# Kernel tuning notes

Measured on AMD Instinct MI355X. Metric: run time of the kernel, lower is better.

Reference implementation:

```python
import jax, jax.numpy as jnp
import numpy as np

WINDOWS = ((0, 8), (4, 12), (8, 16))  # DARM.SEG_WINDOWS
TOPK = 2                               # DARM.TOPK_SEG_PAIRS


def _l2norm(x, axis=-1, eps=1e-12):
    # torch F.normalize: x / max(||x||, eps)
    n = jnp.linalg.norm(x, axis=axis, keepdims=True)
    return x / jnp.maximum(n, eps)


def _segments(x):
    # x: [B, T, D] -> [B, W, L, D]
    return jnp.stack([x[:, s:e, :] for s, e in WINDOWS], axis=1)


def setup_inputs() -> dict:
    key = jax.random.key(0)
    k1, k2 = jax.random.split(key)
    n_way, n_shot, n_query, T, D = 10, 5, 400, 16, 1024
    support_features = jax.random.normal(k1, (n_way * n_shot, T, D), dtype=jnp.float32)
    query_features = jax.random.normal(k2, (n_query, T, D), dtype=jnp.float32)
    # init weights [0.5, 0.5] -> log -> softmax == softmax(zeros)
    fusion_logits = jnp.zeros((2,), dtype=jnp.float32)
    return {
        "support_features": support_features,
        "query_features": query_features,
        "fusion_logits": fusion_logits,
        "n_way": n_way,
        "n_shot": n_shot,
    }


def reference(support_features, query_features, fusion_logits, n_way, n_shot):
    # support_features: [C*K, T, D] with labels repeat(arange(C), K) (sorted, balanced)
    C, K = n_way, n_shot
    Q, T, D = query_features.shape
    inv_sqrt_d = 1.0 / np.sqrt(D).astype(np.float32)

    # ---- global branch: bi-MHM over class prototypes ----
    proto = support_features.reshape(C, K, T, D).mean(axis=1)          # [C, T, D]
    qn = _l2norm(query_features)                                       # [Q, T, D]
    pn = _l2norm(proto)                                                # [C, T, D]
    sim = jnp.einsum("qtd,csd->qcts", qn, pn)                          # [Q, C, T, T]
    dist = 1.0 - sim
    global_dist = dist.min(axis=3).sum(axis=2) + dist.min(axis=2).sum(axis=2)  # [Q, C]
    global_score = -global_dist

    # ---- segment branch ----
    sup_seg = _segments(support_features)                              # [C*K, W, L, D]
    q_seg = _segments(query_features)                                  # [Q, W, L, D]
    W, L = q_seg.shape[1], q_seg.shape[2]
    # group support by class: [C, W, K*L, D]
    cls_sup = sup_seg.reshape(C, K, W, L, D).transpose(0, 2, 1, 3, 4).reshape(C, W, K * L, D)

    sup_cond = _l2norm(cls_sup.mean(axis=2))                           # [C, W, D]
    q_cond = _l2norm(q_seg.mean(axis=2))                               # [Q, W, D]

    # attention-pool support tokens conditioned on each query segment mean
    s_scores = jnp.einsum("cwnd,qvd->qcvwn", cls_sup, q_cond) * inv_sqrt_d
    s_attn = jax.nn.softmax(s_scores, axis=-1)
    pooled_sup = jnp.einsum("qcvwn,cwnd->qcvwd", s_attn, cls_sup)      # [Q, C, W, W, D]
    # cosine(query_cond, pooled_sup); query_cond already unit norm
    score_s2q = jnp.einsum("qvd,qcvwd->qcvw", q_cond, _l2norm(pooled_sup))

    # attention-pool query tokens conditioned on each support segment mean
    q_scores = jnp.einsum("qvnd,cwd->qcvwn", q_seg, sup_cond) * inv_sqrt_d
    q_attn = jax.nn.softmax(q_scores, axis=-1)
    pooled_q = jnp.einsum("qcvwn,qvnd->qcvwd", q_attn, q_seg)          # [Q, C, W, W, D]
    score_q2s = jnp.einsum("qcvwd,cwd->qcvw", _l2norm(pooled_q), sup_cond)

    k = min(TOPK, W * W)
    top_s2q = jax.lax.top_k(score_s2q.reshape(Q, C, W * W), k)[0].mean(axis=-1)
    top_q2s = jax.lax.top_k(score_q2s.reshape(Q, C, W * W), k)[0].mean(axis=-1)
    segment_score = 0.5 * (top_s2q + top_q2s)                          # [Q, C]

    fusion = jax.nn.softmax(fusion_logits)
    final_logits = fusion[0] * global_score + fusion[1] * segment_score
    return final_logits
```

## Files before the change

### kernel.cpp

```cpp
#include <hip/hip_runtime.h>
#include <math.h>

#define C_WAY 10
#define K_SHOT 5
#define T_LEN 16
#define D_DIM 1024
#define NW 3
#define SEG_L 8

typedef __attribute__((ext_vector_type(8))) __bf16 bf16x8;
typedef __attribute__((ext_vector_type(4))) float f32x4;

static inline int cdiv(int a, int b) { return (a + b - 1) / b; }

__device__ __forceinline__ unsigned short f2bf(float f) {
    unsigned int u = __float_as_uint(f);
    u += 0x7fffu + ((u >> 16) & 1u);
    return (unsigned short)(u >> 16);
}
__device__ __forceinline__ float bf2f(unsigned short b) {
    return __uint_as_float(((unsigned int)b) << 16);
}
__device__ __forceinline__ ushort4 f2bf4(float4 v) {
    ushort4 b = {f2bf(v.x), f2bf(v.y), f2bf(v.z), f2bf(v.w)};
    return b;
}

__device__ __forceinline__ float wsum(float v) {
#pragma unroll
    for (int o = 32; o; o >>= 1) v += __shfl_xor(v, o);
    return v;
}
__device__ __forceinline__ float wmax(float v) {
#pragma unroll
    for (int o = 32; o; o >>= 1) v = fmaxf(v, __shfl_xor(v, o));
    return v;
}
__device__ __forceinline__ float wsum8(float v) {
#pragma unroll
    for (int o = 4; o; o >>= 1) v += __shfl_xor(v, o);
    return v;
}
__device__ __forceinline__ float wmax8(float v) {
#pragma unroll
    for (int o = 4; o; o >>= 1) v = fmaxf(v, __shfl_xor(v, o));
    return v;
}

__device__ __forceinline__ int cls_row(int i) {
    int c = i / 120, rem = i - c * 120;
    int w = rem / 40, tok = rem - w * 40;
    return c * 80 + (tok >> 3) * 16 + w * 4 + (tok & 7);
}
__device__ __forceinline__ int qseg_row(int m) {
    int q = m / 24, rem = m - q * 24;
    return q * 16 + (rem >> 3) * 4 + (rem & 7);
}

__global__ __launch_bounds__(256) void k_prep(const float* __restrict__ sup,
                                              const float* __restrict__ query,
                                              unsigned short* __restrict__ qbf,
                                              float* __restrict__ qrow_inv,
                                              unsigned short* __restrict__ qcondbf,
                                              unsigned short* __restrict__ supbf,
                                              unsigned short* __restrict__ protobf,
                                              float* __restrict__ pn_inv,
                                              unsigned short* __restrict__ scondbf,
                                              int Q) {
    __shared__ float red[NW][4];
    int b = blockIdx.x;
    int t = threadIdx.x, wv = t >> 6, lane = t & 63;
    if (b < Q) {
        int qq = b;
#pragma unroll
        for (int r0 = 0; r0 < 4; ++r0) {
            int row = qq * T_LEN + wv * 4 + r0;
            float sq = 0.f;
#pragma unroll
            for (int i = 0; i < 4; ++i) {
                float4 v = *(const float4*)&query[(size_t)row * D_DIM + (i * 64 + lane) * 4];
                *(ushort4*)&qbf[(size_t)row * D_DIM + (i * 64 + lane) * 4] = f2bf4(v);
                sq += v.x * v.x + v.y * v.y + v.z * v.z + v.w * v.w;
            }
            sq = wsum(sq);
            if (lane == 0) qrow_inv[row] = 1.0f / fmaxf(sqrtf(sq), 1e-12f);
        }
        __syncthreads();
        for (int v = 0; v < NW; ++v) {
            float4 acc = {0.f, 0.f, 0.f, 0.f};
#pragma unroll
            for (int l = 0; l < SEG_L; ++l) {
                ushort4 bb = *(const ushort4*)&qbf[((size_t)(qq * T_LEN + v * 4 + l)) * D_DIM + t * 4];
                acc.x += bf2f(bb.x); acc.y += bf2f(bb.y); acc.z += bf2f(bb.z); acc.w += bf2f(bb.w);
            }
            acc.x *= 0.125f; acc.y *= 0.125f; acc.z *= 0.125f; acc.w *= 0.125f;
            float sq = acc.x * acc.x + acc.y * acc.y + acc.z * acc.z + acc.w * acc.w;
            sq = wsum(sq);
            if (lane == 0) red[v][wv] = sq;
            __syncthreads();
            float tot = red[v][0] + red[v][1] + red[v][2] + red[v][3];
            float scl = 1.0f / fmaxf(sqrtf(tot), 1e-12f);
            float4 o = {acc.x * scl, acc.y * scl, acc.z * scl, acc.w * scl};
            *(ushort4*)&qcondbf[((size_t)(qq * NW + v)) * D_DIM + t * 4] = f2bf4(o);
            __syncthreads();
        }
    } else if (b < Q + C_WAY * K_SHOT) {
        int s = b - Q;
#pragma unroll
        for (int i = 0; i < 16; ++i) {
            int qd = i * 256 + t;
            float4 v = *(const float4*)&sup[(size_t)s * 16384 + qd * 4];
            *(ushort4*)&supbf[(size_t)s * 16384 + qd * 4] = f2bf4(v);
        }
    } else {
        int c = b - Q - C_WAY * K_SHOT;
#pragma unroll
        for (int r0 = 0; r0 < 4; ++r0) {
            int tt = wv * 4 + r0;
            float4 a[4] = {};
            for (int k = 0; k < K_SHOT; ++k)
#pragma unroll
                for (int i = 0; i < 4; ++i) {
                    float4 v = *(const float4*)&sup[((size_t)(c * 80 + k * 16 + tt)) * D_DIM + (i * 64 + lane) * 4];
                    a[i].x += v.x; a[i].y += v.y; a[i].z += v.z; a[i].w += v.w;
                }
            float sq = 0.f;
#pragma unroll
            for (int i = 0; i < 4; ++i) {
                a[i].x *= 0.2f; a[i].y *= 0.2f; a[i].z *= 0.2f; a[i].w *= 0.2f;
                sq += a[i].x * a[i].x + a[i].y * a[i].y + a[i].z * a[i].z + a[i].w * a[i].w;
            }
            sq = wsum(sq);
            if (lane == 0) pn_inv[c * T_LEN + tt] = 1.0f / fmaxf(sqrtf(sq), 1e-12f);
#pragma unroll
            for (int i = 0; i < 4; ++i)
                *(ushort4*)&protobf[((size_t)(c * T_LEN + tt)) * D_DIM + (i * 64 + lane) * 4] = f2bf4(a[i]);
        }
        if (wv < NW) {
            float4 a[4] = {};
            for (int k = 0; k < K_SHOT; ++k)
#pragma unroll
                for (int l = 0; l < SEG_L; ++l)
#pragma unroll
                    for (int i = 0; i < 4; ++i) {
                        float4 v = *(const float4*)&sup[((size_t)(c * 80 + k * 16 + wv * 4 + l)) * D_DIM + (i * 64 + lane) * 4];
                        a[i].x += v.x; a[i].y += v.y; a[i].z += v.z; a[i].w += v.w;
                    }
            float sq = 0.f;
            const float s = 1.0f / 40.0f;
#pragma unroll
            for (int i = 0; i < 4; ++i) {
                a[i].x *= s; a[i].y *= s; a[i].z *= s; a[i].w *= s;
                sq += a[i].x * a[i].x + a[i].y * a[i].y + a[i].z * a[i].z + a[i].w * a[i].w;
            }
            sq = wsum(sq);
            float scl = 1.0f / fmaxf(sqrtf(sq), 1e-12f);
#pragma unroll
            for (int i = 0; i < 4; ++i) {
                float4 o = {a[i].x * scl, a[i].y * scl, a[i].z * scl, a[i].w * scl};
                *(ushort4*)&scondbf[((size_t)(c * NW + wv)) * D_DIM + (i * 64 + lane) * 4] = f2bf4(o);
            }
        }
    }
}

template <int AM, int BM>
__device__ __forceinline__ void gemm_tile(const unsigned short* __restrict__ A,
                                          const unsigned short* __restrict__ B,
                                          float* __restrict__ Cb,
                                          int M, int N, int m0, int n0, int batch,
                                          unsigned short (&As)[64][72],
                                          unsigned short (&Bs)[64][72]) {
    int t = threadIdx.x;
    int srow = t >> 2, sk = (t & 3) * 8;
    long ga = -1, gb = -1;
    int am = m0 + srow;
    if (am < M) ga = (AM == 0) ? am : (AM == 1 ? qseg_row(am) : cls_row(batch * 40 + am));
    int bn = n0 + srow;
    if (bn < N) gb = (BM == 0) ? bn : (BM == 1 ? cls_row(bn) : cls_row(batch * 40 + bn));

    int w = t >> 6, l = t & 63;
    int rowbase = (w >> 1) * 32, colbase = (w & 1) * 32;
    int fr = l & 15, fc = l >> 4;

    f32x4 acc[2][2] = {};
    uint4 ra0 = {0, 0, 0, 0}, ra1 = {0, 0, 0, 0}, rb0 = {0, 0, 0, 0}, rb1 = {0, 0, 0, 0};
    if (ga >= 0) {
        ra0 = *(const uint4*)&A[(size_t)ga * D_DIM + sk];
        ra1 = *(const uint4*)&A[(size_t)ga * D_DIM + sk + 32];
    }
    if (gb >= 0) {
        rb0 = *(const uint4*)&B[(size_t)gb * D_DIM + sk];
        rb1 = *(const uint4*)&B[(size_t)gb * D_DIM + sk + 32];
    }
    for (int k0 = 0; k0 < D_DIM; k0 += 64) {
        __syncthreads();
        *(uint4*)&As[srow][sk] = ra0;
        *(uint4*)&As[srow][sk + 32] = ra1;
        *(uint4*)&Bs[srow][sk] = rb0;
        *(uint4*)&Bs[srow][sk + 32] = rb1;
        __syncthreads();
        int kn = k0 + 64;
        if (kn < D_DIM) {
            if (ga >= 0) {
                ra0 = *(const uint4*)&A[(size_t)ga * D_DIM + kn + sk];
                ra1 = *(const uint4*)&A[(size_t)ga * D_DIM + kn + sk + 32];
            }
            if (gb >= 0) {
                rb0 = *(const uint4*)&B[(size_t)gb * D_DIM + kn + sk];
                rb1 = *(const uint4*)&B[(size_t)gb * D_DIM + kn + sk + 32];
            }
        }
#pragma unroll
        for (int kk = 0; kk < 2; ++kk) {
            bf16x8 a0 = *(const bf16x8*)&As[rowbase + fr][kk * 32 + fc * 8];
            bf16x8 a1 = *(const bf16x8*)&As[rowbase + 16 + fr][kk * 32 + fc * 8];
            bf16x8 b0 = *(const bf16x8*)&Bs[colbase + fr][kk * 32 + fc * 8];
            bf16x8 b1 = *(const bf16x8*)&Bs[colbase + 16 + fr][kk * 32 + fc * 8];
            acc[0][0] = __builtin_amdgcn_mfma_f32_16x16x32_bf16(a0, b0, acc[0][0], 0, 0, 0);
            acc[0][1] = __builtin_amdgcn_mfma_f32_16x16x32_bf16(a0, b1, acc[0][1], 0, 0, 0);
            acc[1][0] = __builtin_amdgcn_mfma_f32_16x16x32_bf16(a1, b0, acc[1][0], 0, 0, 0);
            acc[1][1] = __builtin_amdgcn_mfma_f32_16x16x32_bf16(a1, b1, acc[1][1], 0, 0, 0);
        }
    }
    int crow = fc * 4, ccol = fr;
#pragma unroll
    for (int fi = 0; fi < 2; ++fi)
#pragma unroll
        for (int fj = 0; fj < 2; ++fj)
#pragma unroll
            for (int j = 0; j < 4; ++j) {
                int m = m0 + rowbase + fi * 16 + crow + j;
                int n = n0 + colbase + fj * 16 + ccol;
                if (m < M && n < N) Cb[(size_t)m * N + n] = acc[fi][fj][j];
            }
}

__global__ __launch_bounds__(256) void k_mega(const unsigned short* __restrict__ qbf,
                                              const unsigned short* __restrict__ protobf,
                                              const unsigned short* __restrict__ qcondbf,
                                              const unsigned short* __restrict__ supbf,
                                              const unsigned short* __restrict__ scondbf,
                                              float* __restrict__ SIM,
                                              float* __restrict__ Sraw,
                                              float* __restrict__ Qraw,
                                              float* __restrict__ Gsup,
                                              float* __restrict__ Gq,
                                              int Q, int mt0, int nb0, int mt1, int nb1,
                                              int nb2, int nb3) {
    __shared__ __align__(16) unsigned short As[64][72];
    __shared__ __align__(16) unsigned short Bs[64][72];
    int bid = blockIdx.x;
    if (bid < nb0) {
        int mtile = bid % mt0, ntile = bid / mt0;
        gemm_tile<0, 0>(qbf, protobf, SIM, Q * T_LEN, 160, mtile * 64, ntile * 64, 0, As, Bs);
    } else if (bid < nb0 + nb1) {
        int b2 = bid - nb0;
        int mtile = b2 % mt1, ntile = b2 / mt1;
        gemm_tile<0, 1>(qcondbf, supbf, Sraw, Q * NW, 1200, mtile * 64, ntile * 64, 0, As, Bs);
    } else if (bid < nb0 + nb1 + nb2) {
        int mtile = bid - nb0 - nb1;
        gemm_tile<1, 0>(qbf, scondbf, Qraw, Q * 24, 30, mtile * 64, 0, 0, As, Bs);
    } else if (bid < nb0 + nb1 + nb2 + nb3) {
        int batch = bid - nb0 - nb1 - nb2;
        gemm_tile<2, 2>(supbf, supbf, Gsup + (size_t)batch * 1600, 40, 40, 0, 0, batch, As, Bs);
    } else {
        int idx = bid - nb0 - nb1 - nb2 - nb3;
        int gw = idx * 4 + (threadIdx.x >> 6);
        int lane = threadIdx.x & 63;
        int QNW = Q * NW;
        int qv0 = gw * 2, qv1 = gw * 2 + 1;
        if (qv0 >= QNW) return;
        int fr = lane & 15, fc = lane >> 4;
        int half = fr >> 3;
        int qv = (half && qv1 < QNW) ? qv1 : qv0;
        int row = (qv / 3) * T_LEN + (qv % 3) * 4 + (fr & 7);
        const unsigned short* src = qbf + (size_t)row * D_DIM + fc * 8;
        f32x4 acc = {};
        for (int k0 = 0; k0 < D_DIM; k0 += 32) {
            bf16x8 f = *(const bf16x8*)&src[k0];
            acc = __builtin_amdgcn_mfma_f32_16x16x32_bf16(f, f, acc, 0, 0, 0);
        }
        if (fr < 8 && fc < 2) {
#pragma unroll
            for (int jj = 0; jj < 4; ++jj)
                Gq[(size_t)qv0 * 64 + (fc * 4 + jj) * 8 + fr] = acc[jj];
        }
        if (fr >= 8 && fc >= 2 && qv1 < QNW) {
#pragma unroll
            for (int jj = 0; jj < 4; ++jj)
                Gq[(size_t)qv1 * 64 + ((fc - 2) * 4 + jj) * 8 + (fr - 8)] = acc[jj];
        }
    }
}

__global__ __launch_bounds__(64) void k_final2(const float* __restrict__ Sraw,
                                               const float* __restrict__ Qraw,
                                               const float* __restrict__ Gsup,
                                               const float* __restrict__ Gq,
                                               const float* __restrict__ SIM,
                                               const float* __restrict__ qrow_inv,
                                               const float* __restrict__ pn_inv,
                                               const float* __restrict__ fusion,
                                               float* __restrict__ out) {
    __shared__ __align__(16) float Gs[1600];
    __shared__ float ebuf[40];
    __shared__ float e8buf[8];
    __shared__ float dtile[16 * 17];
    __shared__ float qi_s[16], pi_s[16];
    int bid = blockIdx.x;
    int q = bid / 10, c = bid % 10;
    int lane = threadIdx.x;
    const float inv_sqrt_d = 0.03125f;

    if (lane < 16) {
        qi_s[lane] = qrow_inv[q * 16 + lane];
        pi_s[lane] = pn_inv[c * 16 + lane];
    }
    __syncthreads();
    {
        int t = lane >> 2, s4 = (lane & 3) * 4;
        float4 sv = *(const float4*)&SIM[((size_t)(q * 16 + t)) * 160 + c * 16 + s4];
        float qi = qi_s[t];
        dtile[t * 17 + s4 + 0] = 1.0f - sv.x * qi * pi_s[s4 + 0];
        dtile[t * 17 + s4 + 1] = 1.0f - sv.y * qi * pi_s[s4 + 1];
        dtile[t * 17 + s4 + 2] = 1.0f - sv.z * qi * pi_s[s4 + 2];
        dtile[t * 17 + s4 + 3] = 1.0f - sv.w * qi * pi_s[s4 + 3];
    }
    __syncthreads();
    float gpart = 0.f;
    if (lane < 16) {
        float mn = 3.4e38f;
#pragma unroll
        for (int s = 0; s < 16; ++s) mn = fminf(mn, dtile[lane * 17 + s]);
        gpart = mn;
    } else if (lane < 32) {
        int s = lane - 16;
        float mn = 3.4e38f;
#pragma unroll
        for (int t = 0; t < 16; ++t) mn = fminf(mn, dtile[t * 17 + s]);
        gpart = mn;
    }
    float gscore = -wsum(gpart);

    float b1s = -3.4e38f, b2s = -3.4e38f, b1q = -3.4e38f, b2q = -3.4e38f;
    for (int w = 0; w < 3; ++w) {
        __syncthreads();
#pragma unroll
        for (int j = 0; j < 25; ++j)
            Gs[j * 64 + lane] = Gsup[(size_t)(c * 3 + w) * 1600 + j * 64 + lane];
        for (int v = 0; v < 3; ++v) {
            __syncthreads();
            bool act = lane < 40;
            float raw = act ? Sraw[((size_t)(q * 3 + v)) * 1200 + (c * 3 + w) * 40 + lane] : 0.f;
            float x = act ? raw * inv_sqrt_d : -3.4e38f;
            float mx = wmax(x);
            float e = act ? __expf(x - mx) : 0.f;
            if (act) ebuf[lane] = e;
            float dot_e = wsum(e * raw);
            bool a8 = lane < 8;
            float qraw = a8 ? Qraw[((size_t)((q * 3 + v) * 8 + lane)) * 30 + c * 3 + w] : 0.f;
            float x8 = a8 ? qraw * inv_sqrt_d : -3.4e38f;
            float mx8 = wmax8(x8);
            float e8 = a8 ? __expf(x8 - mx8) : 0.f;
            if (a8) e8buf[lane] = e8;
            float dot8 = wsum8(e8 * qraw);
            __syncthreads();
            float acc = 0.f;
#pragma unroll
            for (int j = 0; j < 25; ++j) {
                int i = j * 64 + lane;
                int m = (i * 52429) >> 21;
                int n = i - m * 40;
                acc = fmaf(ebuf[m] * ebuf[n], Gs[i], acc);
            }
            float quad = wsum(acc);
            float sc = dot_e / sqrtf(quad);
            int mm = lane >> 3, nn = lane & 7;
            float q2 = e8buf[mm] * e8buf[nn] * Gq[(size_t)(q * 3 + v) * 64 + lane];
            q2 = wsum(q2);
            float sc8 = __shfl(dot8, 0) / sqrtf(q2);
            if (sc > b1s) { b2s = b1s; b1s = sc; } else if (sc > b2s) b2s = sc;
            if (sc8 > b1q) { b2q = b1q; b1q = sc8; } else if (sc8 > b2q) b2q = sc8;
        }
    }
    if (lane == 0) {
        float seg = 0.5f * (0.5f * (b1s + b2s) + 0.5f * (b1q + b2q));
        float l0 = fusion[0], l1 = fusion[1];
        float mmx = fmaxf(l0, l1);
        float e0 = __expf(l0 - mmx), e1 = __expf(l1 - mmx);
        float f0 = e0 / (e0 + e1), f1 = e1 / (e0 + e1);
        out[bid] = f0 * gscore + f1 * seg;
    }
}

extern "C" void kernel_launch(void* const* d_in, const int* in_sizes, int n_in,
                              void* d_out, int out_size, void* d_ws, size_t ws_size,
                              hipStream_t stream) {
    const float* sup = (const float*)d_in[0];
    const float* query = (const float*)d_in[1];
    const float* fusion = (const float*)d_in[2];
    float* out = (float*)d_out;
    const int Q = in_sizes[1] / (T_LEN * D_DIM);

    float* w = (float*)d_ws;
    size_t off = 0;
    unsigned short* qbf = (unsigned short*)(w + off);     off += (size_t)Q * T_LEN * D_DIM / 2;
    unsigned short* supbf = (unsigned short*)(w + off);   off += (size_t)C_WAY * K_SHOT * T_LEN * D_DIM / 2;
    unsigned short* protobf = (unsigned short*)(w + off); off += (size_t)C_WAY * T_LEN * D_DIM / 2;
    unsigned short* qcondbf = (unsigned short*)(w + off); off += (size_t)Q * NW * D_DIM / 2;
    unsigned short* scondbf = (unsigned short*)(w + off); off += (size_t)C_WAY * NW * D_DIM / 2 + 8;
    float* pn_inv = w + off;    off += C_WAY * T_LEN;
    float* qrow_inv = w + off;  off += (size_t)Q * T_LEN;
    float* Gsup = w + off;      off += C_WAY * NW * 40 * 40;
    float* Gq = w + off;        off += (size_t)Q * NW * 64;
    float* SIM = w + off;       off += (size_t)Q * T_LEN * C_WAY * T_LEN;
    float* Sraw = w + off;      off += (size_t)Q * NW * C_WAY * NW * 40;
    float* Qraw = w + off;      off += (size_t)Q * NW * SEG_L * C_WAY * NW;
    (void)ws_size; (void)n_in; (void)out_size;

    k_prep<<<Q + C_WAY * K_SHOT + C_WAY, 256, 0, stream>>>(
        sup, query, qbf, qrow_inv, qcondbf, supbf, protobf, pn_inv, scondbf, Q);

    int mt0 = cdiv(Q * T_LEN, 64), nb0 = mt0 * cdiv(160, 64);
    int mt1 = cdiv(Q * NW, 64), nb1 = mt1 * cdiv(1200, 64);
    int nb2 = cdiv(Q * 24, 64);
    int nb3 = C_WAY * NW;
    int ngq = cdiv(Q * NW, 8);
    k_mega<<<nb0 + nb1 + nb2 + nb3 + ngq, 256, 0, stream>>>(
        qbf, protobf, qcondbf, supbf, scondbf, SIM, Sraw, Qraw, Gsup, Gq,
        Q, mt0, nb0, mt1, nb1, nb2, nb3);

    k_final2<<<Q * C_WAY, 64, 0, stream>>>(Sraw, Qraw, Gsup, Gq, SIM, qrow_inv, pn_inv,
                                           fusion, out);
}
```

Before: 75.33 us.

## Fuse global min-sum into GEMM epilogue, enlarge tiles, parallelize final kernel

```diff
diff --git a/kernel.cpp b/kernel.cpp
--- a/kernel.cpp
+++ b/kernel.cpp
@@ -164,76 +164,121 @@
     }
 }
 
-template <int AM, int BM>
+template <int AM, int BM, bool EPI>
 __device__ __forceinline__ void gemm_tile(const unsigned short* __restrict__ A,
                                           const unsigned short* __restrict__ B,
                                           float* __restrict__ Cb,
                                           int M, int N, int m0, int n0, int batch,
-                                          unsigned short (&As)[64][72],
-                                          unsigned short (&Bs)[64][72]) {
+                                          unsigned short (&As)[128][72],
+                                          unsigned short (&Bs)[64][72],
+                                          const float* __restrict__ qrow_inv,
+                                          const float* __restrict__ pn_inv,
+                                          float* __restrict__ gscore,
+                                          float (&qis)[128], float (&pis)[64]) {
     int t = threadIdx.x;
-    int srow = t >> 2, sk = (t & 3) * 8;
+    int arow_l = t >> 1, au = t & 1;
+    int brow_l = t >> 2, bu = t & 3;
     long ga = -1, gb = -1;
-    int am = m0 + srow;
+    int am = m0 + arow_l;
     if (am < M) ga = (AM == 0) ? am : (AM == 1 ? qseg_row(am) : cls_row(batch * 40 + am));
-    int bn = n0 + srow;
+    int bn = n0 + brow_l;
     if (bn < N) gb = (BM == 0) ? bn : (BM == 1 ? cls_row(bn) : cls_row(batch * 40 + bn));
 
     int w = t >> 6, l = t & 63;
-    int rowbase = (w >> 1) * 32, colbase = (w & 1) * 32;
+    int rowbase = (w >> 1) * 64, colbase = (w & 1) * 32;
     int fr = l & 15, fc = l >> 4;
 
-    f32x4 acc[2][2] = {};
-    uint4 ra0 = {0, 0, 0, 0}, ra1 = {0, 0, 0, 0}, rb0 = {0, 0, 0, 0}, rb1 = {0, 0, 0, 0};
+    if (EPI) {
+        if (t < 128) qis[t] = qrow_inv[m0 + t];
+        else if (t < 192) pis[t - 128] = (n0 + t - 128 < N) ? pn_inv[n0 + t - 128] : 0.f;
+    }
+
+    f32x4 acc[4][2] = {};
+    uint4 ra[4] = {}, rb[2] = {};
     if (ga >= 0) {
-        ra0 = *(const uint4*)&A[(size_t)ga * D_DIM + sk];
-        ra1 = *(const uint4*)&A[(size_t)ga * D_DIM + sk + 32];
+#pragma unroll
+        for (int i = 0; i < 4; ++i) ra[i] = *(const uint4*)&A[(size_t)ga * D_DIM + (au + 2 * i) * 8];
     }
     if (gb >= 0) {
-        rb0 = *(const uint4*)&B[(size_t)gb * D_DIM + sk];
-        rb1 = *(const uint4*)&B[(size_t)gb * D_DIM + sk + 32];
+#pragma unroll
+        for (int i = 0; i < 2; ++i) rb[i] = *(const uint4*)&B[(size_t)gb * D_DIM + (bu + 4 * i) * 8];
     }
     for (int k0 = 0; k0 < D_DIM; k0 += 64) {
         __syncthreads();
-        *(uint4*)&As[srow][sk] = ra0;
-        *(uint4*)&As[srow][sk + 32] = ra1;
-        *(uint4*)&Bs[srow][sk] = rb0;
-        *(uint4*)&Bs[srow][sk + 32] = rb1;
+#pragma unroll
+        for (int i = 0; i < 4; ++i) *(uint4*)&As[arow_l][(au + 2 * i) * 8] = ra[i];
+#pragma unroll
+        for (int i = 0; i < 2; ++i) *(uint4*)&Bs[brow_l][(bu + 4 * i) * 8] = rb[i];
         __syncthreads();
         int kn = k0 + 64;
         if (kn < D_DIM) {
             if (ga >= 0) {
-                ra0 = *(const uint4*)&A[(size_t)ga * D_DIM + kn + sk];
-                ra1 = *(const uint4*)&A[(size_t)ga * D_DIM + kn + sk + 32];
+#pragma unroll
+                for (int i = 0; i < 4; ++i) ra[i] = *(const uint4*)&A[(size_t)ga * D_DIM + kn + (au + 2 * i) * 8];
             }
             if (gb >= 0) {
-                rb0 = *(const uint4*)&B[(size_t)gb * D_DIM + kn + sk];
-                rb1 = *(const uint4*)&B[(size_t)gb * D_DIM + kn + sk + 32];
+#pragma unroll
+                for (int i = 0; i < 2; ++i) rb[i] = *(const uint4*)&B[(size_t)gb * D_DIM + kn + (bu + 4 * i) * 8];
             }
         }
 #pragma unroll
         for (int kk = 0; kk < 2; ++kk) {
-            bf16x8 a0 = *(const bf16x8*)&As[rowbase + fr][kk * 32 + fc * 8];
-            bf16x8 a1 = *(const bf16x8*)&As[rowbase + 16 + fr][kk * 32 + fc * 8];
             bf16x8 b0 = *(const bf16x8*)&Bs[colbase + fr][kk * 32 + fc * 8];
             bf16x8 b1 = *(const bf16x8*)&Bs[colbase + 16 + fr][kk * 32 + fc * 8];
-            acc[0][0] = __builtin_amdgcn_mfma_f32_16x16x32_bf16(a0, b0, acc[0][0], 0, 0, 0);
-            acc[0][1] = __builtin_amdgcn_mfma_f32_16x16x32_bf16(a0, b1, acc[0][1], 0, 0, 0);
-            acc[1][0] = __builtin_amdgcn_mfma_f32_16x16x32_bf16(a1, b0, acc[1][0], 0, 0, 0);
-            acc[1][1] = __builtin_amdgcn_mfma_f32_16x16x32_bf16(a1, b1, acc[1][1], 0, 0, 0);
-        }
-    }
-    int crow = fc * 4, ccol = fr;
-#pragma unroll
-    for (int fi = 0; fi < 2; ++fi)
-#pragma unroll
-        for (int fj = 0; fj < 2; ++fj)
-#pragma unroll
-            for (int j = 0; j < 4; ++j) {
-                int m = m0 + rowbase + fi * 16 + crow + j;
-                int n = n0 + colbase + fj * 16 + ccol;
-                if (m < M && n < N) Cb[(size_t)m * N + n] = acc[fi][fj][j];
-            }
+#pragma unroll
+            for (int fi = 0; fi < 4; ++fi) {
+                bf16x8 a = *(const bf16x8*)&As[rowbase + fi * 16 + fr][kk * 32 + fc * 8];
+                acc[fi][0] = __builtin_amdgcn_mfma_f32_16x16x32_bf16(a, b0, acc[fi][0], 0, 0, 0);
+                acc[fi][1] = __builtin_amdgcn_mfma_f32_16x16x32_bf16(a, b1, acc[fi][1], 0, 0, 0);
+            }
+        }
+    }
+    if (EPI) {
+#pragma unroll
+        for (int fi = 0; fi < 4; ++fi) {
+            float qi[4];
+#pragma unroll
+            for (int j = 0; j < 4; ++j) qi[j] = qis[rowbase + fi * 16 + fc * 4 + j];
+#pragma unroll
+            for (int fj = 0; fj < 2; ++fj) {
+                int nc = n0 + colbase + fj * 16;
+                if (nc >= N) continue;
+                float pi = pis[colbase + fj * 16 + fr];
+                float dd[4], rm[4];
+#pragma unroll
+                for (int j = 0; j < 4; ++j) { dd[j] = 1.0f - acc[fi][fj][j] * qi[j] * pi; rm[j] = dd[j]; }
+#pragma unroll
+                for (int o = 1; o <= 8; o <<= 1)
+#pragma unroll
+                    for (int j = 0; j < 4; ++j) rm[j] = fminf(rm[j], __shfl_xor(rm[j], o));
+                float rowsum = rm[0] + rm[1] + rm[2] + rm[3];
+                rowsum += __shfl_xor(rowsum, 16);
+                rowsum += __shfl_xor(rowsum, 32);
+                float cm = fminf(fminf(dd[0], dd[1]), fminf(dd[2], dd[3]));
+                cm = fminf(cm, __shfl_xor(cm, 16));
+                cm = fminf(cm, __shfl_xor(cm, 32));
+                float colsum = cm;
+#pragma unroll
+                for (int o = 1; o <= 8; o <<= 1) colsum += __shfl_xor(colsum, o);
+                if (l == 0) {
+                    int qq = (m0 + rowbase) / 16 + fi, cc = nc / 16;
+                    gscore[qq * C_WAY + cc] = -(rowsum + colsum);
+                }
+            }
+        }
+    } else {
+        int crow = fc * 4, ccol = fr;
+#pragma unroll
+        for (int fi = 0; fi < 4; ++fi)
+#pragma unroll
+            for (int fj = 0; fj < 2; ++fj)
+#pragma unroll
+                for (int j = 0; j < 4; ++j) {
+                    int m = m0 + rowbase + fi * 16 + crow + j;
+                    int n = n0 + colbase + fj * 16 + ccol;
+                    if (m < M && n < N) Cb[(size_t)m * N + n] = acc[fi][fj][j];
+                }
+    }
 }
 
 __global__ __launch_bounds__(256) void k_mega(const unsigned short* __restrict__ qbf,
@@ -241,29 +286,37 @@
                                               const unsigned short* __restrict__ qcondbf,
                                               const unsigned short* __restrict__ supbf,
                                               const unsigned short* __restrict__ scondbf,
-                                              float* __restrict__ SIM,
+                                              const float* __restrict__ qrow_inv,
+                                              const float* __restrict__ pn_inv,
+                                              float* __restrict__ gscore,
                                               float* __restrict__ Sraw,
                                               float* __restrict__ Qraw,
                                               float* __restrict__ Gsup,
                                               float* __restrict__ Gq,
                                               int Q, int mt0, int nb0, int mt1, int nb1,
                                               int nb2, int nb3) {
-    __shared__ __align__(16) unsigned short As[64][72];
+    __shared__ __align__(16) unsigned short As[128][72];
     __shared__ __align__(16) unsigned short Bs[64][72];
+    __shared__ float qis[128];
+    __shared__ float pis[64];
     int bid = blockIdx.x;
     if (bid < nb0) {
         int mtile = bid % mt0, ntile = bid / mt0;
-        gemm_tile<0, 0>(qbf, protobf, SIM, Q * T_LEN, 160, mtile * 64, ntile * 64, 0, As, Bs);
+        gemm_tile<0, 0, true>(qbf, protobf, nullptr, Q * T_LEN, 160, mtile * 128, ntile * 64, 0,
+                              As, Bs, qrow_inv, pn_inv, gscore, qis, pis);
     } else if (bid < nb0 + nb1) {
         int b2 = bid - nb0;
         int mtile = b2 % mt1, ntile = b2 / mt1;
-        gemm_tile<0, 1>(qcondbf, supbf, Sraw, Q * NW, 1200, mtile * 64, ntile * 64, 0, As, Bs);
+        gemm_tile<0, 1, false>(qcondbf, supbf, Sraw, Q * NW, 1200, mtile * 128, ntile * 64, 0,
+                               As, Bs, nullptr, nullptr, nullptr, qis, pis);
     } else if (bid < nb0 + nb1 + nb2) {
         int mtile = bid - nb0 - nb1;
-        gemm_tile<1, 0>(qbf, scondbf, Qraw, Q * 24, 30, mtile * 64, 0, 0, As, Bs);
+        gemm_tile<1, 0, false>(qbf, scondbf, Qraw, Q * 24, 30, mtile * 128, 0, 0,
+                               As, Bs, nullptr, nullptr, nullptr, qis, pis);
     } else if (bid < nb0 + nb1 + nb2 + nb3) {
         int batch = bid - nb0 - nb1 - nb2;
-        gemm_tile<2, 2>(supbf, supbf, Gsup + (size_t)batch * 1600, 40, 40, 0, 0, batch, As, Bs);
+        gemm_tile<2, 2, false>(supbf, supbf, Gsup + (size_t)batch * 1600, 40, 40, 0, 0, batch,
+                               As, Bs, nullptr, nullptr, nullptr, qis, pis);
     } else {
         int idx = bid - nb0 - nb1 - nb2 - nb3;
         int gw = idx * 4 + (threadIdx.x >> 6);
@@ -294,103 +347,76 @@
     }
 }
 
-__global__ __launch_bounds__(64) void k_final2(const float* __restrict__ Sraw,
-                                               const float* __restrict__ Qraw,
-                                               const float* __restrict__ Gsup,
-                                               const float* __restrict__ Gq,
-                                               const float* __restrict__ SIM,
-                                               const float* __restrict__ qrow_inv,
-                                               const float* __restrict__ pn_inv,
-                                               const float* __restrict__ fusion,
-                                               float* __restrict__ out) {
-    __shared__ __align__(16) float Gs[1600];
-    __shared__ float ebuf[40];
-    __shared__ float e8buf[8];
-    __shared__ float dtile[16 * 17];
-    __shared__ float qi_s[16], pi_s[16];
+__global__ __launch_bounds__(192) void k_final3(const float* __restrict__ Sraw,
+                                                const float* __restrict__ Qraw,
+                                                const float* __restrict__ Gsup,
+                                                const float* __restrict__ Gq,
+                                                const float* __restrict__ gscore,
+                                                const float* __restrict__ fusion,
+                                                float* __restrict__ out) {
+    __shared__ __align__(16) float Gs[3][1600];
+    __shared__ float ebuf[3][40];
+    __shared__ float e8buf[3][8];
+    __shared__ float s2q_all[9], q2s_all[9];
     int bid = blockIdx.x;
     int q = bid / 10, c = bid % 10;
-    int lane = threadIdx.x;
+    int w = threadIdx.x >> 6, lane = threadIdx.x & 63;
     const float inv_sqrt_d = 0.03125f;
 
-    if (lane < 16) {
-        qi_s[lane] = qrow_inv[q * 16 + lane];
-        pi_s[lane] = pn_inv[c * 16 + lane];
+    const float* Gp = &Gsup[(size_t)(c * 3 + w) * 1600];
+#pragma unroll
+    for (int j = 0; j < 25; ++j) Gs[w][j * 64 + lane] = Gp[j * 64 + lane];
+
+    for (int v = 0; v < 3; ++v) {
+        bool act = lane < 40;
+        float raw = act ? Sraw[((size_t)(q * 3 + v)) * 1200 + (c * 3 + w) * 40 + lane] : 0.f;
+        float x = act ? raw * inv_sqrt_d : -3.4e38f;
+        float mx = wmax(x);
+        float e = act ? __expf(x - mx) : 0.f;
+        if (act) ebuf[w][lane] = e;
+        float dot_e = wsum(e * raw);
+        bool a8 = lane < 8;
+        float qraw = a8 ? Qraw[((size_t)((q * 3 + v) * 8 + lane)) * 30 + c * 3 + w] : 0.f;
+        float x8 = a8 ? qraw * inv_sqrt_d : -3.4e38f;
+        float mx8 = wmax8(x8);
+        float e8 = a8 ? __expf(x8 - mx8) : 0.f;
+        if (a8) e8buf[w][lane] = e8;
+        float dot8 = wsum8(e8 * qraw);
+        float acc = 0.f;
+#pragma unroll
+        for (int j = 0; j < 25; ++j) {
+            int i = j * 64 + lane;
+            int m = (i * 52429) >> 21;
+            int n = i - m * 40;
+            acc = fmaf(ebuf[w][m] * ebuf[w][n], Gs[w][i], acc);
+        }
+        float quad = wsum(acc);
+        float sc = dot_e / sqrtf(quad);
+        int mm = lane >> 3, nn = lane & 7;
+        float q2 = e8buf[w][mm] * e8buf[w][nn] * Gq[(size_t)(q * 3 + v) * 64 + lane];
+        q2 = wsum(q2);
+        float sc8 = __shfl(dot8, 0) / sqrtf(q2);
+        if (lane == 0) {
+            s2q_all[w * 3 + v] = sc;
+            q2s_all[w * 3 + v] = sc8;
+        }
     }
     __syncthreads();
-    {
-        int t = lane >> 2, s4 = (lane & 3) * 4;
-        float4 sv = *(const float4*)&SIM[((size_t)(q * 16 + t)) * 160 + c * 16 + s4];
-        float qi = qi_s[t];
-        dtile[t * 17 + s4 + 0] = 1.0f - sv.x * qi * pi_s[s4 + 0];
-        dtile[t * 17 + s4 + 1] = 1.0f - sv.y * qi * pi_s[s4 + 1];
-        dtile[t * 17 + s4 + 2] = 1.0f - sv.z * qi * pi_s[s4 + 2];
-        dtile[t * 17 + s4 + 3] = 1.0f - sv.w * qi * pi_s[s4 + 3];
-    }
-    __syncthreads();
-    float gpart = 0.f;
-    if (lane < 16) {
-        float mn = 3.4e38f;
-#pragma unroll
-        for (int s = 0; s < 16; ++s) mn = fminf(mn, dtile[lane * 17 + s]);
-        gpart = mn;
-    } else if (lane < 32) {
-        int s = lane - 16;
-        float mn = 3.4e38f;
-#pragma unroll
-        for (int t = 0; t < 16; ++t) mn = fminf(mn, dtile[t * 17 + s]);
-        gpart = mn;
-    }
-    float gscore = -wsum(gpart);
-
-    float b1s = -3.4e38f, b2s = -3.4e38f, b1q = -3.4e38f, b2q = -3.4e38f;
-    for (int w = 0; w < 3; ++w) {
-        __syncthreads();
-#pragma unroll
-        for (int j = 0; j < 25; ++j)
-            Gs[j * 64 + lane] = Gsup[(size_t)(c * 3 + w) * 1600 + j * 64 + lane];
-        for (int v = 0; v < 3; ++v) {
-            __syncthreads();
-            bool act = lane < 40;
-            float raw = act ? Sraw[((size_t)(q * 3 + v)) * 1200 + (c * 3 + w) * 40 + lane] : 0.f;
-            float x = act ? raw * inv_sqrt_d : -3.4e38f;
-            float mx = wmax(x);
-            float e = act ? __expf(x - mx) : 0.f;
-            if (act) ebuf[lane] = e;
-            float dot_e = wsum(e * raw);
-            bool a8 = lane < 8;
-            float qraw = a8 ? Qraw[((size_t)((q * 3 + v) * 8 + lane)) * 30 + c * 3 + w] : 0.f;
-            float x8 = a8 ? qraw * inv_sqrt_d : -3.4e38f;
-            float mx8 = wmax8(x8);
-            float e8 = a8 ? __expf(x8 - mx8) : 0.f;
-            if (a8) e8buf[lane] = e8;
-            float dot8 = wsum8(e8 * qraw);
-            __syncthreads();
-            float acc = 0.f;
-#pragma unroll
-            for (int j = 0; j < 25; ++j) {
-                int i = j * 64 + lane;
-                int m = (i * 52429) >> 21;
-                int n = i - m * 40;
-                acc = fmaf(ebuf[m] * ebuf[n], Gs[i], acc);
-            }
-            float quad = wsum(acc);
-            float sc = dot_e / sqrtf(quad);
-            int mm = lane >> 3, nn = lane & 7;
-            float q2 = e8buf[mm] * e8buf[nn] * Gq[(size_t)(q * 3 + v) * 64 + lane];
-            q2 = wsum(q2);
-            float sc8 = __shfl(dot8, 0) / sqrtf(q2);
-            if (sc > b1s) { b2s = b1s; b1s = sc; } else if (sc > b2s) b2s = sc;
-            if (sc8 > b1q) { b2q = b1q; b1q = sc8; } else if (sc8 > b2q) b2q = sc8;
-        }
-    }
-    if (lane == 0) {
+    if (threadIdx.x == 0) {
+        float b1s = -3.4e38f, b2s = -3.4e38f, b1q = -3.4e38f, b2q = -3.4e38f;
+#pragma unroll
+        for (int i = 0; i < 9; ++i) {
+            float s = s2q_all[i];
+            if (s > b1s) { b2s = b1s; b1s = s; } else if (s > b2s) b2s = s;
+            float qq2 = q2s_all[i];
+            if (qq2 > b1q) { b2q = b1q; b1q = qq2; } else if (qq2 > b2q) b2q = qq2;
+        }
         float seg = 0.5f * (0.5f * (b1s + b2s) + 0.5f * (b1q + b2q));
         float l0 = fusion[0], l1 = fusion[1];
         float mmx = fmaxf(l0, l1);
         float e0 = __expf(l0 - mmx), e1 = __expf(l1 - mmx);
         float f0 = e0 / (e0 + e1), f1 = e1 / (e0 + e1);
-        out[bid] = f0 * gscore + f1 * seg;
+        out[bid] = f0 * gscore[bid] + f1 * seg;
     }
 }
 
@@ -412,9 +438,9 @@
     unsigned short* scondbf = (unsigned short*)(w + off); off += (size_t)C_WAY * NW * D_DIM / 2 + 8;
     float* pn_inv = w + off;    off += C_WAY * T_LEN;
     float* qrow_inv = w + off;  off += (size_t)Q * T_LEN;
+    float* gscore = w + off;    off += (size_t)Q * C_WAY;
     float* Gsup = w + off;      off += C_WAY * NW * 40 * 40;
     float* Gq = w + off;        off += (size_t)Q * NW * 64;
-    float* SIM = w + off;       off += (size_t)Q * T_LEN * C_WAY * T_LEN;
     float* Sraw = w + off;      off += (size_t)Q * NW * C_WAY * NW * 40;
     float* Qraw = w + off;      off += (size_t)Q * NW * SEG_L * C_WAY * NW;
     (void)ws_size; (void)n_in; (void)out_size;
@@ -422,15 +448,14 @@
     k_prep<<<Q + C_WAY * K_SHOT + C_WAY, 256, 0, stream>>>(
         sup, query, qbf, qrow_inv, qcondbf, supbf, protobf, pn_inv, scondbf, Q);
 
-    int mt0 = cdiv(Q * T_LEN, 64), nb0 = mt0 * cdiv(160, 64);
-    int mt1 = cdiv(Q * NW, 64), nb1 = mt1 * cdiv(1200, 64);
-    int nb2 = cdiv(Q * 24, 64);
+    int mt0 = cdiv(Q * T_LEN, 128), nb0 = mt0 * cdiv(160, 64);
+    int mt1 = cdiv(Q * NW, 128), nb1 = mt1 * cdiv(1200, 64);
+    int nb2 = cdiv(Q * 24, 128);
     int nb3 = C_WAY * NW;
     int ngq = cdiv(Q * NW, 8);
     k_mega<<<nb0 + nb1 + nb2 + nb3 + ngq, 256, 0, stream>>>(
-        qbf, protobf, qcondbf, supbf, scondbf, SIM, Sraw, Qraw, Gsup, Gq,
-        Q, mt0, nb0, mt1, nb1, nb2, nb3);
-
-    k_final2<<<Q * C_WAY, 64, 0, stream>>>(Sraw, Qraw, Gsup, Gq, SIM, qrow_inv, pn_inv,
-                                           fusion, out);
-}
+        qbf, protobf, qcondbf, supbf, scondbf, qrow_inv, pn_inv, gscore,
+        Sraw, Qraw, Gsup, Gq, Q, mt0, nb0, mt1, nb1, nb2, nb3);
+
+    k_final3<<<Q * C_WAY, 192, 0, stream>>>(Sraw, Qraw, Gsup, Gq, gscore, fusion, out);
+}
```

After: 111.5 us. 48.0% more time.
